# Kernel tuning notes

Hardware: AMD Instinct MI355X
Metric: run time of the kernel (lower is better)

The kernel has to match this reference:

```python
import jax, jax.numpy as jnp
import numpy as np

B, T, C, HD = 4, 2048, 1024, 64

def setup_inputs() -> dict:
    key = jax.random.key(0)
    kx, kq, kk, kv = jax.random.split(key, 4)
    # Weights stored as [n_embed, head_size]; equivalent to torch Linear weight transposed.
    scale = 1.0 / np.sqrt(C)
    return {
        "x": jax.random.normal(kx, (B, T, C), dtype=jnp.float32),
        "Wq": jax.random.normal(kq, (C, HD), dtype=jnp.float32) * scale,
        "Wk": jax.random.normal(kk, (C, HD), dtype=jnp.float32) * scale,
        "Wv": jax.random.normal(kv, (C, HD), dtype=jnp.float32) * scale,
    }

def reference(x, Wq, Wk, Wv):
    # Projections (no bias)
    q = x @ Wq  # [B,T,HD]
    k = x @ Wk
    v = x @ Wv
    hd = k.shape[-1]
    # NOTE: original multiplies by sqrt(head_size) (not the usual 1/sqrt) -- faithful.
    scores = jnp.einsum("btd,bsd->bts", q, k) * (hd ** 0.5)  # [B,T,T]
    # First softmax over full (unmasked) rows
    w = jax.nn.softmax(scores, axis=-1)
    # Causal mask applied AFTER the first softmax, then a second softmax
    causal = jnp.tril(jnp.ones((q.shape[1], q.shape[1]), dtype=bool))  # [T,T]
    w = jnp.where(causal[None, :, :], w, -jnp.inf)
    w = jax.nn.softmax(w, axis=-1)
    out = jnp.einsum("bts,bsd->btd", w, v)  # [B,T,HD]
    return out
```

## Files before the change

### kernel.cpp

```cpp
#include <hip/hip_runtime.h>
#include <math.h>

#define T_  2048
#define C_  1024
#define HD_ 64

typedef __attribute__((ext_vector_type(8))) short bf16x8;
typedef __attribute__((ext_vector_type(4))) float f32x4;

#define MFMA_BF16(A, B, C) __builtin_amdgcn_mfma_f32_16x16x32_bf16(A, B, C, 0, 0, 0)

__device__ __forceinline__ short f2bf(float f) {
    union { float f; unsigned u; } v; v.f = f;
    unsigned r = v.u + 0x7fffu + ((v.u >> 16) & 1u);
    return (short)(r >> 16);
}
__device__ __forceinline__ float bf2f(short s) {
    union { float f; unsigned u; } v;
    v.u = ((unsigned)(unsigned short)s) << 16;
    return v.f;
}

__global__ __launch_bounds__(256) void prep_w_kernel(
    const float* __restrict__ Wq, const float* __restrict__ Wk,
    const float* __restrict__ Wv, short* __restrict__ wt)
{
    const int m = blockIdx.y;
    const float* W = (m == 0) ? Wq : (m == 1) ? Wk : Wv;
    const int t = threadIdx.x;
    const int c = blockIdx.x * 64 + (t >> 2);
    const int hg = (t & 3) * 16;
    const float4* wp = (const float4*)(W + (size_t)c * HD_ + hg);
    short* hi = wt + (size_t)(m * 2 + 0) * 64 * 1024;
    short* lo = wt + (size_t)(m * 2 + 1) * 64 * 1024;
    #pragma unroll
    for (int u = 0; u < 4; ++u) {
        float4 f = wp[u];
        float vs[4] = {f.x, f.y, f.z, f.w};
        #pragma unroll
        for (int e = 0; e < 4; ++e) {
            int h = hg + u * 4 + e;
            short hh = f2bf(vs[e]);
            hi[(size_t)h * 1024 + c] = hh;
            lo[(size_t)h * 1024 + c] = f2bf(vs[e] - bf2f(hh));
        }
    }
}

__global__ __launch_bounds__(256) void qkv_proj_kernel(
    const float* __restrict__ x, const short* __restrict__ wt,
    short* __restrict__ qhp, short* __restrict__ qlp,
    short* __restrict__ khp, short* __restrict__ klp,
    short* __restrict__ vtp)
{
    __shared__ __align__(16) short xh[32 * 64], xl[32 * 64];
    __shared__ __align__(16) short wh[192 * 64], wl[192 * 64];

    const int t = threadIdx.x, L = t & 63, wv = t >> 6;
    const int R0 = blockIdx.x * 32;
    const int xrow = t >> 3, xch = t & 7;

    f32x4 acc[2][3];
    #pragma unroll
    for (int i = 0; i < 2; ++i)
        #pragma unroll
        for (int j = 0; j < 3; ++j) acc[i][j] = {0.f, 0.f, 0.f, 0.f};

    float4 xa0, xa1;
    bf16x8 wr[2][6];
    const float* xp = x + (size_t)(R0 + xrow) * C_ + xch * 8;

    auto loadX = [&](int c0) {
        xa0 = *(const float4*)(xp + c0);
        xa1 = *(const float4*)(xp + c0 + 4);
    };
    auto loadW = [&](int c0) {
        #pragma unroll
        for (int pl = 0; pl < 2; ++pl)
            #pragma unroll
            for (int u = 0; u < 6; ++u) {
                int cc = t + 256 * u;
                int row = cc >> 3, ch = cc & 7;
                int m = row >> 6, h = row & 63;
                wr[pl][u] = *(const bf16x8*)(wt + (size_t)(m * 2 + pl) * 65536
                                             + (size_t)h * 1024 + c0 + ch * 8);
            }
    };

    loadX(0); loadW(0);
    for (int c0 = 0; c0 < C_; c0 += 64) {
        __syncthreads();
        {
            float vs[8] = {xa0.x, xa0.y, xa0.z, xa0.w, xa1.x, xa1.y, xa1.z, xa1.w};
            bf16x8 vh, vl;
            #pragma unroll
            for (int e = 0; e < 8; ++e) {
                short hh = f2bf(vs[e]);
                vh[e] = hh;
                vl[e] = f2bf(vs[e] - bf2f(hh));
            }
            int slot = (xch ^ (xrow & 7)) * 8;
            *(bf16x8*)&xh[xrow * 64 + slot] = vh;
            *(bf16x8*)&xl[xrow * 64 + slot] = vl;
        }
        {
            #pragma unroll
            for (int pl = 0; pl < 2; ++pl)
                #pragma unroll
                for (int u = 0; u < 6; ++u) {
                    int cc = t + 256 * u;
                    int row = cc >> 3, ch = cc & 7;
                    short* dst = pl ? wl : wh;
                    *(bf16x8*)&dst[row * 64 + ((ch ^ (row & 7)) * 8)] = wr[pl][u];
                }
        }
        if (c0 + 64 < C_) { loadX(c0 + 64); loadW(c0 + 64); }
        __syncthreads();
        #pragma unroll
        for (int kc = 0; kc < 2; ++kc) {
            const int ch = kc * 4 + (L >> 4);
            bf16x8 axh[2], axl[2], bwh[3], bwl[3];
            #pragma unroll
            for (int rt = 0; rt < 2; ++rt) {
                int row = rt * 16 + (L & 15);
                int off = row * 64 + ((ch ^ (row & 7)) * 8);
                axh[rt] = *(const bf16x8*)&xh[off];
                axl[rt] = *(const bf16x8*)&xl[off];
            }
            #pragma unroll
            for (int cl = 0; cl < 3; ++cl) {
                int ct = wv + cl * 4;
                int wrow = ct * 16 + (L & 15);
                int off = wrow * 64 + ((ch ^ (wrow & 7)) * 8);
                bwh[cl] = *(const bf16x8*)&wh[off];
                bwl[cl] = *(const bf16x8*)&wl[off];
            }
            #pragma unroll
            for (int rt = 0; rt < 2; ++rt) {
                acc[rt][0] = MFMA_BF16(axl[rt], bwh[0], acc[rt][0]);
                acc[rt][0] = MFMA_BF16(axh[rt], bwl[0], acc[rt][0]);
                acc[rt][0] = MFMA_BF16(axh[rt], bwh[0], acc[rt][0]);
                acc[rt][1] = MFMA_BF16(axl[rt], bwh[1], acc[rt][1]);
                acc[rt][1] = MFMA_BF16(axh[rt], bwl[1], acc[rt][1]);
                acc[rt][1] = MFMA_BF16(axh[rt], bwh[1], acc[rt][1]);
                acc[rt][2] = MFMA_BF16(bwh[2], axh[rt], acc[rt][2]);
            }
        }
    }

    const int quad = L >> 4;
    #pragma unroll
    for (int rt = 0; rt < 2; ++rt) {
        #pragma unroll
        for (int r = 0; r < 4; ++r) {
            int row = R0 + rt * 16 + quad * 4 + r;
            int h = wv * 16 + (L & 15);
            float vq = acc[rt][0][r] * 8.f;
            short hq = f2bf(vq);
            qhp[(size_t)row * HD_ + h] = hq;
            qlp[(size_t)row * HD_ + h] = f2bf(vq - bf2f(hq));
            float vk = acc[rt][1][r];
            short hk = f2bf(vk);
            khp[(size_t)row * HD_ + h] = hk;
            klp[(size_t)row * HD_ + h] = f2bf(vk - bf2f(hk));
            int d = wv * 16 + quad * 4 + r;
            int tt = R0 + rt * 16 + (L & 15);
            int bb = tt >> 11, tl = tt & (T_ - 1);
            vtp[(size_t)(bb * 64 + d) * T_ + tl] = f2bf(acc[rt][2][r]);
        }
    }
}

__global__ __launch_bounds__(256) void stats_kernel(
    const short* __restrict__ qhp, const short* __restrict__ qlp,
    const short* __restrict__ khp, const short* __restrict__ klp,
    float* __restrict__ pm, float* __restrict__ sc)
{
    __shared__ __align__(16) short khs[64 * 64], kls[64 * 64];
    __shared__ float red[4 * 64 * 2];

    const int t = threadIdx.x, L = t & 63, wv = t >> 6;
    const int bt = blockIdx.x, seg = blockIdx.y, b = blockIdx.z;
    const int R0 = bt * 64, S0 = seg * 256;

    bf16x8 qfh[4][2], qfl[4][2];
    #pragma unroll
    for (int rt = 0; rt < 4; ++rt)
        #pragma unroll
        for (int dc = 0; dc < 2; ++dc) {
            int row = R0 + rt * 16 + (L & 15);
            size_t off = ((size_t)b * T_ + row) * HD_ + dc * 32 + (L >> 4) * 8;
            qfh[rt][dc] = *(const bf16x8*)(qhp + off);
            qfl[rt][dc] = *(const bf16x8*)(qlp + off);
        }

    float ml[4][4], ll[4][4];
    #pragma unroll
    for (int rt = 0; rt < 4; ++rt)
        #pragma unroll
        for (int r = 0; r < 4; ++r) { ml[rt][r] = -1e30f; ll[rt][r] = 0.f; }

    const int pl = t >> 7, id = t & 127;
    const short* ksrc = pl ? klp : khp;
    short* kdst = pl ? kls : khs;
    bf16x8 kr[4];
    auto loadK = [&](int jt) {
        #pragma unroll
        for (int u = 0; u < 4; ++u) {
            int cid = id * 4 + u;
            int col = cid >> 3, ch = cid & 7;
            kr[u] = *(const bf16x8*)(ksrc
                + ((size_t)b * T_ + S0 + jt * 64 + col) * HD_ + ch * 8);
        }
    };

    loadK(0);
    for (int jt = 0; jt < 4; ++jt) {
        __syncthreads();
        #pragma unroll
        for (int u = 0; u < 4; ++u) {
            int cid = id * 4 + u;
            int col = cid >> 3, ch = cid & 7;
            *(bf16x8*)&kdst[col * 64 + ((ch ^ (col & 7)) * 8)] = kr[u];
        }
        __syncthreads();
        if (jt < 3) loadK(jt + 1);
        const int colL = wv * 16 + (L & 15);
        bf16x8 kf[2], kfl[2];
        #pragma unroll
        for (int dc = 0; dc < 2; ++dc) {
            int ch = dc * 4 + (L >> 4);
            int off = colL * 64 + ((ch ^ (colL & 7)) * 8);
            kf[dc]  = *(const bf16x8*)&khs[off];
            kfl[dc] = *(const bf16x8*)&kls[off];
        }
        const bool doStore = (S0 + jt * 64) <= (R0 + 63);
        #pragma unroll
        for (int rt = 0; rt < 4; ++rt) {
            f32x4 s = {0.f, 0.f, 0.f, 0.f};
            #pragma unroll
            for (int dc = 0; dc < 2; ++dc) {
                s = MFMA_BF16(qfl[rt][dc], kf[dc], s);
                s = MFMA_BF16(qfh[rt][dc], kfl[dc], s);
                s = MFMA_BF16(qfh[rt][dc], kf[dc], s);
            }
            if (doStore) {
                #pragma unroll
                for (int r = 0; r < 4; ++r) {
                    int row = R0 + rt * 16 + (L >> 4) * 4 + r;
                    sc[((size_t)b * T_ + row) * T_ + S0 + jt * 64 + colL] = s[r];
                }
            }
            #pragma unroll
            for (int r = 0; r < 4; ++r) {
                float mn = fmaxf(ml[rt][r], s[r]);
                ll[rt][r] = ll[rt][r] * __expf(ml[rt][r] - mn) + __expf(s[r] - mn);
                ml[rt][r] = mn;
            }
        }
    }
    #pragma unroll
    for (int off = 1; off < 16; off <<= 1)
        #pragma unroll
        for (int rt = 0; rt < 4; ++rt)
            #pragma unroll
            for (int r = 0; r < 4; ++r) {
                float mo = __shfl_xor(ml[rt][r], off, 64);
                float lo = __shfl_xor(ll[rt][r], off, 64);
                float mn = fmaxf(ml[rt][r], mo);
                ll[rt][r] = ll[rt][r] * __expf(ml[rt][r] - mn) + lo * __expf(mo - mn);
                ml[rt][r] = mn;
            }
    if ((L & 15) == 0) {
        #pragma unroll
        for (int rt = 0; rt < 4; ++rt)
            #pragma unroll
            for (int r = 0; r < 4; ++r) {
                int row = rt * 16 + (L >> 4) * 4 + r;
                red[(wv * 64 + row) * 2 + 0] = ml[rt][r];
                red[(wv * 64 + row) * 2 + 1] = ll[rt][r];
            }
    }
    __syncthreads();
    if (t < 64) {
        float M = red[t * 2], S = red[t * 2 + 1];
        #pragma unroll
        for (int w = 1; w < 4; ++w) {
            float mo = red[(w * 64 + t) * 2], lo = red[(w * 64 + t) * 2 + 1];
            float mn = fmaxf(M, mo);
            S = S * __expf(M - mn) + lo * __expf(mo - mn);
            M = mn;
        }
        size_t o = ((size_t)((b * 32 + bt) * 8 + seg) * 64 + t) * 2;
        pm[o] = M;
        pm[o + 1] = S;
    }
}

__global__ __launch_bounds__(256) void stat_merge_kernel(
    const float* __restrict__ pm, float* __restrict__ msp, float* __restrict__ ilp)
{
    int gid = blockIdx.x * 256 + threadIdx.x;
    int b = gid >> 11, rl = gid & 2047, bt = rl >> 6, rr = rl & 63;
    float M = -1e30f, S = 0.f;
    #pragma unroll
    for (int seg = 0; seg < 8; ++seg) {
        size_t o = ((size_t)((b * 32 + bt) * 8 + seg) * 64 + rr) * 2;
        float mo = pm[o], lo = pm[o + 1];
        float mn = fmaxf(M, mo);
        S = S * __expf(M - mn) + lo * __expf(mo - mn);
        M = mn;
    }
    msp[gid] = M;
    ilp[gid] = 1.f / S;
}

__global__ __launch_bounds__(256) void pv_kernel(
    const float* __restrict__ sc, const short* __restrict__ vtp,
    const float* __restrict__ msp, const float* __restrict__ ilp,
    float* __restrict__ out)
{
    __shared__ float ored[4][16][64];
    __shared__ float dred[4][16];

    const int t = threadIdx.x, L = t & 63, wv = t >> 6;
    const int b = blockIdx.x & 3;
    const int p = 127 - (blockIdx.x >> 2);
    const int T0 = p * 16;
    const int row = T0 + (L & 15);

    const float ms = msp[b * T_ + row];
    const float is = ilp[b * T_ + row];
    const float* srow = sc + ((size_t)b * T_ + row) * T_;
    const short* vb = vtp + (size_t)b * 64 * T_;
    const int nJ = (T0 + 143) >> 7;
    const int cq = (L >> 4) * 8;

    f32x4 ov[4];
    #pragma unroll
    for (int dt = 0; dt < 4; ++dt) ov[dt] = {0.f, 0.f, 0.f, 0.f};
    float dn = 0.f;

    for (int jt = 0; jt < nJ; ++jt) {
        const int c0 = jt * 128 + wv * 32 + cq;
        float4 s0 = *(const float4*)(srow + c0);
        float4 s1 = *(const float4*)(srow + c0 + 4);
        float vs[8] = {s0.x, s0.y, s0.z, s0.w, s1.x, s1.y, s1.z, s1.w};
        bf16x8 ef;
        #pragma unroll
        for (int e = 0; e < 8; ++e) {
            float pvv = __expf(vs[e] - ms) * is;
            float evv = (c0 + e <= row) ? __expf(pvv) : 0.f;
            dn += evv;
            ef[e] = f2bf(evv);
        }
        #pragma unroll
        for (int dt = 0; dt < 4; ++dt) {
            bf16x8 vf = *(const bf16x8*)(vb + (size_t)(dt * 16 + (L & 15)) * T_ + c0);
            ov[dt] = MFMA_BF16(ef, vf, ov[dt]);
        }
    }

    dn += __shfl_xor(dn, 16, 64);
    dn += __shfl_xor(dn, 32, 64);
    if (L < 16) dred[wv][L] = dn;
    #pragma unroll
    for (int dt = 0; dt < 4; ++dt)
        #pragma unroll
        for (int r = 0; r < 4; ++r)
            ored[wv][(L >> 4) * 4 + r][dt * 16 + (L & 15)] = ov[dt][r];
    __syncthreads();

    const int orow = t >> 4, d0 = (t & 15) * 4;
    float D = dred[0][orow] + dred[1][orow] + dred[2][orow] + dred[3][orow];
    float di = 1.f / D;
    float4 o;
    o.x = (ored[0][orow][d0 + 0] + ored[1][orow][d0 + 0]
         + ored[2][orow][d0 + 0] + ored[3][orow][d0 + 0]) * di;
    o.y = (ored[0][orow][d0 + 1] + ored[1][orow][d0 + 1]
         + ored[2][orow][d0 + 1] + ored[3][orow][d0 + 1]) * di;
    o.z = (ored[0][orow][d0 + 2] + ored[1][orow][d0 + 2]
         + ored[2][orow][d0 + 2] + ored[3][orow][d0 + 2]) * di;
    o.w = (ored[0][orow][d0 + 3] + ored[1][orow][d0 + 3]
         + ored[2][orow][d0 + 3] + ored[3][orow][d0 + 3]) * di;
    *(float4*)(out + ((size_t)b * T_ + T0 + orow) * HD_ + d0) = o;
}

extern "C" void kernel_launch(void* const* d_in, const int* in_sizes, int n_in,
                              void* d_out, int out_size, void* d_ws, size_t ws_size,
                              hipStream_t stream) {
    (void)in_sizes; (void)n_in; (void)out_size; (void)ws_size;
    const float* x  = (const float*)d_in[0];
    const float* Wq = (const float*)d_in[1];
    const float* Wk = (const float*)d_in[2];
    const float* Wv = (const float*)d_in[3];
    float* outp = (float*)d_out;

    char* ws = (char*)d_ws;
    short* wt  = (short*)ws;
    float* pm  = (float*)ws;
    float* msp = (float*)(ws + 524288);
    float* ilp = (float*)(ws + 557056);
    short* qh = (short*)(ws + 786432);
    short* ql = (short*)(ws + 786432 + 1048576);
    short* kh = (short*)(ws + 786432 + 2 * 1048576);
    short* kl = (short*)(ws + 786432 + 3 * 1048576);
    short* vt = (short*)(ws + 786432 + 4 * 1048576);
    float* sc = (float*)(ws + 8388608);

    prep_w_kernel<<<dim3(16, 3), 256, 0, stream>>>(Wq, Wk, Wv, wt);
    qkv_proj_kernel<<<dim3(256), 256, 0, stream>>>(x, wt, qh, ql, kh, kl, vt);
    stats_kernel<<<dim3(32, 8, 4), 256, 0, stream>>>(qh, ql, kh, kl, pm, sc);
    stat_merge_kernel<<<dim3(32), 256, 0, stream>>>(pm, msp, ilp);
    pv_kernel<<<dim3(512), 256, 0, stream>>>(sc, vt, msp, ilp, outp);
}
```

Measured before the change: 148.9 us.

## Pre-swizzle weights into MFMA fragment layout, drop LDS staging, fuse stat merge

Weights are pre-laid out in prep_w into per-lane MFMA fragment order, so the projection kernel loads them straight into registers with 512 threads and no LDS weight tile. The stats kernel reads K fragments directly from global memory with double-buffered registers, which removes the LDS staging and its barriers. The separate stat-merge kernel is folded into pv_kernel, which saves one launch, and pv blocks are reordered to balance causal work. The cost is more global traffic from redundant fragment loads and higher register pressure.

```diff
diff --git a/kernel.cpp b/kernel.cpp
--- a/kernel.cpp
+++ b/kernel.cpp
@@ -23,151 +23,138 @@
 
 __global__ __launch_bounds__(256) void prep_w_kernel(
     const float* __restrict__ Wq, const float* __restrict__ Wk,
-    const float* __restrict__ Wv, short* __restrict__ wt)
+    const float* __restrict__ Wv, short* __restrict__ wtf)
 {
     const int m = blockIdx.y;
     const float* W = (m == 0) ? Wq : (m == 1) ? Wk : Wv;
     const int t = threadIdx.x;
     const int c = blockIdx.x * 64 + (t >> 2);
     const int hg = (t & 3) * 16;
+    const int ct = m * 4 + (t & 3);
+    const int c0i = c >> 6, kc = (c >> 5) & 1, lq = (c >> 3) & 3, e = c & 7;
     const float4* wp = (const float4*)(W + (size_t)c * HD_ + hg);
-    short* hi = wt + (size_t)(m * 2 + 0) * 64 * 1024;
-    short* lo = wt + (size_t)(m * 2 + 1) * 64 * 1024;
     #pragma unroll
     for (int u = 0; u < 4; ++u) {
         float4 f = wp[u];
         float vs[4] = {f.x, f.y, f.z, f.w};
         #pragma unroll
-        for (int e = 0; e < 4; ++e) {
-            int h = hg + u * 4 + e;
-            short hh = f2bf(vs[e]);
-            hi[(size_t)h * 1024 + c] = hh;
-            lo[(size_t)h * 1024 + c] = f2bf(vs[e] - bf2f(hh));
-        }
-    }
-}
-
-__global__ __launch_bounds__(256) void qkv_proj_kernel(
-    const float* __restrict__ x, const short* __restrict__ wt,
+        for (int ei = 0; ei < 4; ++ei) {
+            int h16 = u * 4 + ei;
+            int L = h16 + 16 * lq;
+            short hh = f2bf(vs[ei]);
+            short lo = f2bf(vs[ei] - bf2f(hh));
+            size_t oh = ((((size_t)(ct * 2 + 0) * 16 + c0i) * 2 + kc) * 64 + L) * 8 + e;
+            size_t ol = ((((size_t)(ct * 2 + 1) * 16 + c0i) * 2 + kc) * 64 + L) * 8 + e;
+            wtf[oh] = hh;
+            wtf[ol] = lo;
+        }
+    }
+}
+
+__global__ __launch_bounds__(512) void qkv_proj_kernel(
+    const float* __restrict__ x, const short* __restrict__ wtf,
     short* __restrict__ qhp, short* __restrict__ qlp,
     short* __restrict__ khp, short* __restrict__ klp,
     short* __restrict__ vtp)
 {
     __shared__ __align__(16) short xh[32 * 64], xl[32 * 64];
-    __shared__ __align__(16) short wh[192 * 64], wl[192 * 64];
 
     const int t = threadIdx.x, L = t & 63, wv = t >> 6;
     const int R0 = blockIdx.x * 32;
-    const int xrow = t >> 3, xch = t & 7;
-
-    f32x4 acc[2][3];
-    #pragma unroll
-    for (int i = 0; i < 2; ++i)
-        #pragma unroll
-        for (int j = 0; j < 3; ++j) acc[i][j] = {0.f, 0.f, 0.f, 0.f};
-
-    float4 xa0, xa1;
-    bf16x8 wr[2][6];
-    const float* xp = x + (size_t)(R0 + xrow) * C_ + xch * 8;
-
-    auto loadX = [&](int c0) {
-        xa0 = *(const float4*)(xp + c0);
-        xa1 = *(const float4*)(xp + c0 + 4);
+    const int rtb = (wv >> 2) * 16;
+    const int ctq = wv & 3;
+
+    f32x4 acc[3];
+    #pragma unroll
+    for (int j = 0; j < 3; ++j) acc[j] = {0.f, 0.f, 0.f, 0.f};
+
+    const int xrow = t >> 4, xc4 = t & 15;
+    const float* xp = x + (size_t)(R0 + xrow) * C_ + xc4 * 4;
+    float4 xa;
+    auto loadX = [&](int c0) { xa = *(const float4*)(xp + c0); };
+
+    const size_t lo8 = (size_t)L * 8;
+    auto loadWF = [&](int c0i, int kc, bf16x8* w) {
+        w[0] = *(const bf16x8*)(wtf + (size_t)((((ctq + 0) * 2 + 0) * 16 + c0i) * 2 + kc) * 512 + lo8);
+        w[1] = *(const bf16x8*)(wtf + (size_t)((((ctq + 0) * 2 + 1) * 16 + c0i) * 2 + kc) * 512 + lo8);
+        w[2] = *(const bf16x8*)(wtf + (size_t)((((ctq + 4) * 2 + 0) * 16 + c0i) * 2 + kc) * 512 + lo8);
+        w[3] = *(const bf16x8*)(wtf + (size_t)((((ctq + 4) * 2 + 1) * 16 + c0i) * 2 + kc) * 512 + lo8);
+        w[4] = *(const bf16x8*)(wtf + (size_t)((((ctq + 8) * 2 + 0) * 16 + c0i) * 2 + kc) * 512 + lo8);
     };
-    auto loadW = [&](int c0) {
-        #pragma unroll
-        for (int pl = 0; pl < 2; ++pl)
-            #pragma unroll
-            for (int u = 0; u < 6; ++u) {
-                int cc = t + 256 * u;
-                int row = cc >> 3, ch = cc & 7;
-                int m = row >> 6, h = row & 63;
-                wr[pl][u] = *(const bf16x8*)(wt + (size_t)(m * 2 + pl) * 65536
-                                             + (size_t)h * 1024 + c0 + ch * 8);
-            }
-    };
-
-    loadX(0); loadW(0);
-    for (int c0 = 0; c0 < C_; c0 += 64) {
+
+    bf16x8 wf0[5], wf1[5];
+    loadX(0);
+    loadWF(0, 0, wf0);
+
+    const int c8 = xc4 >> 1, xhalf = xc4 & 1;
+    const int arow = rtb + (L & 15);
+
+    for (int c0i = 0; c0i < 16; ++c0i) {
         __syncthreads();
         {
-            float vs[8] = {xa0.x, xa0.y, xa0.z, xa0.w, xa1.x, xa1.y, xa1.z, xa1.w};
-            bf16x8 vh, vl;
-            #pragma unroll
-            for (int e = 0; e < 8; ++e) {
+            float vs[4] = {xa.x, xa.y, xa.z, xa.w};
+            short4 vh, vl;
+            short* vhp = (short*)&vh; short* vlp = (short*)&vl;
+            #pragma unroll
+            for (int e = 0; e < 4; ++e) {
                 short hh = f2bf(vs[e]);
-                vh[e] = hh;
-                vl[e] = f2bf(vs[e] - bf2f(hh));
-            }
-            int slot = (xch ^ (xrow & 7)) * 8;
-            *(bf16x8*)&xh[xrow * 64 + slot] = vh;
-            *(bf16x8*)&xl[xrow * 64 + slot] = vl;
-        }
+                vhp[e] = hh;
+                vlp[e] = f2bf(vs[e] - bf2f(hh));
+            }
+            int slot = xrow * 64 + ((c8 ^ (xrow & 7)) * 8) + xhalf * 4;
+            *(short4*)&xh[slot] = vh;
+            *(short4*)&xl[slot] = vl;
+        }
+        if (c0i < 15) loadX((c0i + 1) * 64);
+        __syncthreads();
+
+        loadWF(c0i, 1, wf1);
         {
-            #pragma unroll
-            for (int pl = 0; pl < 2; ++pl)
-                #pragma unroll
-                for (int u = 0; u < 6; ++u) {
-                    int cc = t + 256 * u;
-                    int row = cc >> 3, ch = cc & 7;
-                    short* dst = pl ? wl : wh;
-                    *(bf16x8*)&dst[row * 64 + ((ch ^ (row & 7)) * 8)] = wr[pl][u];
-                }
-        }
-        if (c0 + 64 < C_) { loadX(c0 + 64); loadW(c0 + 64); }
-        __syncthreads();
-        #pragma unroll
-        for (int kc = 0; kc < 2; ++kc) {
-            const int ch = kc * 4 + (L >> 4);
-            bf16x8 axh[2], axl[2], bwh[3], bwl[3];
-            #pragma unroll
-            for (int rt = 0; rt < 2; ++rt) {
-                int row = rt * 16 + (L & 15);
-                int off = row * 64 + ((ch ^ (row & 7)) * 8);
-                axh[rt] = *(const bf16x8*)&xh[off];
-                axl[rt] = *(const bf16x8*)&xl[off];
-            }
-            #pragma unroll
-            for (int cl = 0; cl < 3; ++cl) {
-                int ct = wv + cl * 4;
-                int wrow = ct * 16 + (L & 15);
-                int off = wrow * 64 + ((ch ^ (wrow & 7)) * 8);
-                bwh[cl] = *(const bf16x8*)&wh[off];
-                bwl[cl] = *(const bf16x8*)&wl[off];
-            }
-            #pragma unroll
-            for (int rt = 0; rt < 2; ++rt) {
-                acc[rt][0] = MFMA_BF16(axl[rt], bwh[0], acc[rt][0]);
-                acc[rt][0] = MFMA_BF16(axh[rt], bwl[0], acc[rt][0]);
-                acc[rt][0] = MFMA_BF16(axh[rt], bwh[0], acc[rt][0]);
-                acc[rt][1] = MFMA_BF16(axl[rt], bwh[1], acc[rt][1]);
-                acc[rt][1] = MFMA_BF16(axh[rt], bwl[1], acc[rt][1]);
-                acc[rt][1] = MFMA_BF16(axh[rt], bwh[1], acc[rt][1]);
-                acc[rt][2] = MFMA_BF16(bwh[2], axh[rt], acc[rt][2]);
-            }
+            int ch = 0 * 4 + (L >> 4);
+            int off = arow * 64 + ((ch ^ (arow & 7)) * 8);
+            bf16x8 axh = *(const bf16x8*)&xh[off];
+            bf16x8 axl = *(const bf16x8*)&xl[off];
+            acc[0] = MFMA_BF16(axl, wf0[0], acc[0]);
+            acc[0] = MFMA_BF16(axh, wf0[1], acc[0]);
+            acc[0] = MFMA_BF16(axh, wf0[0], acc[0]);
+            acc[1] = MFMA_BF16(axl, wf0[2], acc[1]);
+            acc[1] = MFMA_BF16(axh, wf0[3], acc[1]);
+            acc[1] = MFMA_BF16(axh, wf0[2], acc[1]);
+            acc[2] = MFMA_BF16(wf0[4], axh, acc[2]);
+        }
+        if (c0i < 15) loadWF(c0i + 1, 0, wf0);
+        {
+            int ch = 1 * 4 + (L >> 4);
+            int off = arow * 64 + ((ch ^ (arow & 7)) * 8);
+            bf16x8 axh = *(const bf16x8*)&xh[off];
+            bf16x8 axl = *(const bf16x8*)&xl[off];
+            acc[0] = MFMA_BF16(axl, wf1[0], acc[0]);
+            acc[0] = MFMA_BF16(axh, wf1[1], acc[0]);
+            acc[0] = MFMA_BF16(axh, wf1[0], acc[0]);
+            acc[1] = MFMA_BF16(axl, wf1[2], acc[1]);
+            acc[1] = MFMA_BF16(axh, wf1[3], acc[1]);
+            acc[1] = MFMA_BF16(axh, wf1[2], acc[1]);
+            acc[2] = MFMA_BF16(wf1[4], axh, acc[2]);
         }
     }
 
     const int quad = L >> 4;
     #pragma unroll
-    for (int rt = 0; rt < 2; ++rt) {
-        #pragma unroll
-        for (int r = 0; r < 4; ++r) {
-            int row = R0 + rt * 16 + quad * 4 + r;
-            int h = wv * 16 + (L & 15);
-            float vq = acc[rt][0][r] * 8.f;
-            short hq = f2bf(vq);
-            qhp[(size_t)row * HD_ + h] = hq;
-            qlp[(size_t)row * HD_ + h] = f2bf(vq - bf2f(hq));
-            float vk = acc[rt][1][r];
-            short hk = f2bf(vk);
-            khp[(size_t)row * HD_ + h] = hk;
-            klp[(size_t)row * HD_ + h] = f2bf(vk - bf2f(hk));
-            int d = wv * 16 + quad * 4 + r;
-            int tt = R0 + rt * 16 + (L & 15);
-            int bb = tt >> 11, tl = tt & (T_ - 1);
-            vtp[(size_t)(bb * 64 + d) * T_ + tl] = f2bf(acc[rt][2][r]);
-        }
+    for (int r = 0; r < 4; ++r) {
+        int row = R0 + rtb + quad * 4 + r;
+        int h = ctq * 16 + (L & 15);
+        float vq = acc[0][r] * 8.f;
+        short hq = f2bf(vq);
+        qhp[(size_t)row * HD_ + h] = hq;
+        qlp[(size_t)row * HD_ + h] = f2bf(vq - bf2f(hq));
+        float vk = acc[1][r];
+        short hk = f2bf(vk);
+        khp[(size_t)row * HD_ + h] = hk;
+        klp[(size_t)row * HD_ + h] = f2bf(vk - bf2f(hk));
+        int d = ctq * 16 + quad * 4 + r;
+        int tt = R0 + rtb + (L & 15);
+        int bb = tt >> 11, tl = tt & (T_ - 1);
+        vtp[(size_t)(bb * 64 + d) * T_ + tl] = f2bf(acc[2][r]);
     }
 }
 
@@ -176,7 +163,6 @@
     const short* __restrict__ khp, const short* __restrict__ klp,
     float* __restrict__ pm, float* __restrict__ sc)
 {
-    __shared__ __align__(16) short khs[64 * 64], kls[64 * 64];
     __shared__ float red[4 * 64 * 2];
 
     const int t = threadIdx.x, L = t & 63, wv = t >> 6;
@@ -200,49 +186,34 @@
         #pragma unroll
         for (int r = 0; r < 4; ++r) { ml[rt][r] = -1e30f; ll[rt][r] = 0.f; }
 
-    const int pl = t >> 7, id = t & 127;
-    const short* ksrc = pl ? klp : khp;
-    short* kdst = pl ? kls : khs;
-    bf16x8 kr[4];
-    auto loadK = [&](int jt) {
-        #pragma unroll
-        for (int u = 0; u < 4; ++u) {
-            int cid = id * 4 + u;
-            int col = cid >> 3, ch = cid & 7;
-            kr[u] = *(const bf16x8*)(ksrc
-                + ((size_t)b * T_ + S0 + jt * 64 + col) * HD_ + ch * 8);
+    const int colL = wv * 16 + (L & 15);
+    const short* kbh = khp + ((size_t)b * T_ + S0 + colL) * HD_;
+    const short* kbl = klp + ((size_t)b * T_ + S0 + colL) * HD_;
+    const int cho = (L >> 4) * 8;
+
+    bf16x8 kfh[2][2], kfl[2][2];
+    auto loadK = [&](int jt, bf16x8 kh[2], bf16x8 kl[2]) {
+        #pragma unroll
+        for (int dc = 0; dc < 2; ++dc) {
+            kh[dc] = *(const bf16x8*)(kbh + (size_t)jt * 64 * HD_ + dc * 32 + cho);
+            kl[dc] = *(const bf16x8*)(kbl + (size_t)jt * 64 * HD_ + dc * 32 + cho);
         }
     };
-
-    loadK(0);
+    loadK(0, kfh[0], kfl[0]);
+
+    #pragma unroll
     for (int jt = 0; jt < 4; ++jt) {
-        __syncthreads();
-        #pragma unroll
-        for (int u = 0; u < 4; ++u) {
-            int cid = id * 4 + u;
-            int col = cid >> 3, ch = cid & 7;
-            *(bf16x8*)&kdst[col * 64 + ((ch ^ (col & 7)) * 8)] = kr[u];
-        }
-        __syncthreads();
-        if (jt < 3) loadK(jt + 1);
-        const int colL = wv * 16 + (L & 15);
-        bf16x8 kf[2], kfl[2];
-        #pragma unroll
-        for (int dc = 0; dc < 2; ++dc) {
-            int ch = dc * 4 + (L >> 4);
-            int off = colL * 64 + ((ch ^ (colL & 7)) * 8);
-            kf[dc]  = *(const bf16x8*)&khs[off];
-            kfl[dc] = *(const bf16x8*)&kls[off];
-        }
+        const int cb = jt & 1;
+        if (jt < 3) loadK(jt + 1, kfh[cb ^ 1], kfl[cb ^ 1]);
         const bool doStore = (S0 + jt * 64) <= (R0 + 63);
         #pragma unroll
         for (int rt = 0; rt < 4; ++rt) {
             f32x4 s = {0.f, 0.f, 0.f, 0.f};
             #pragma unroll
             for (int dc = 0; dc < 2; ++dc) {
-                s = MFMA_BF16(qfl[rt][dc], kf[dc], s);
-                s = MFMA_BF16(qfh[rt][dc], kfl[dc], s);
-                s = MFMA_BF16(qfh[rt][dc], kf[dc], s);
+                s = MFMA_BF16(qfl[rt][dc], kfh[cb][dc], s);
+                s = MFMA_BF16(qfh[rt][dc], kfl[cb][dc], s);
+                s = MFMA_BF16(qfh[rt][dc], kfh[cb][dc], s);
             }
             if (doStore) {
                 #pragma unroll
@@ -297,40 +268,40 @@
     }
 }
 
-__global__ __launch_bounds__(256) void stat_merge_kernel(
-    const float* __restrict__ pm, float* __restrict__ msp, float* __restrict__ ilp)
-{
-    int gid = blockIdx.x * 256 + threadIdx.x;
-    int b = gid >> 11, rl = gid & 2047, bt = rl >> 6, rr = rl & 63;
-    float M = -1e30f, S = 0.f;
-    #pragma unroll
-    for (int seg = 0; seg < 8; ++seg) {
-        size_t o = ((size_t)((b * 32 + bt) * 8 + seg) * 64 + rr) * 2;
-        float mo = pm[o], lo = pm[o + 1];
-        float mn = fmaxf(M, mo);
-        S = S * __expf(M - mn) + lo * __expf(mo - mn);
-        M = mn;
-    }
-    msp[gid] = M;
-    ilp[gid] = 1.f / S;
-}
-
 __global__ __launch_bounds__(256) void pv_kernel(
     const float* __restrict__ sc, const short* __restrict__ vtp,
-    const float* __restrict__ msp, const float* __restrict__ ilp,
-    float* __restrict__ out)
+    const float* __restrict__ pm, float* __restrict__ out)
 {
     __shared__ float ored[4][16][64];
     __shared__ float dred[4][16];
+    __shared__ float msl[16], isl[16];
 
     const int t = threadIdx.x, L = t & 63, wv = t >> 6;
     const int b = blockIdx.x & 3;
-    const int p = 127 - (blockIdx.x >> 2);
+    const int i = blockIdx.x >> 2;
+    const int p = (i < 64) ? (127 - i) : (i - 64);
     const int T0 = p * 16;
+
+    if (t < 16) {
+        int row = T0 + t;
+        int bt = row >> 6, rr = row & 63;
+        float M = -1e30f, S = 0.f;
+        #pragma unroll
+        for (int seg = 0; seg < 8; ++seg) {
+            size_t o = ((size_t)((b * 32 + bt) * 8 + seg) * 64 + rr) * 2;
+            float mo = pm[o], lo = pm[o + 1];
+            float mn = fmaxf(M, mo);
+            S = S * __expf(M - mn) + lo * __expf(mo - mn);
+            M = mn;
+        }
+        msl[t] = M;
+        isl[t] = 1.f / S;
+    }
+    __syncthreads();
+
     const int row = T0 + (L & 15);
-
-    const float ms = msp[b * T_ + row];
-    const float is = ilp[b * T_ + row];
+    const float ms = msl[L & 15];
+    const float is = isl[L & 15];
     const float* srow = sc + ((size_t)b * T_ + row) * T_;
     const short* vb = vtp + (size_t)b * 64 * T_;
     const int nJ = (T0 + 143) >> 7;
@@ -399,8 +370,6 @@
     char* ws = (char*)d_ws;
     short* wt  = (short*)ws;
     float* pm  = (float*)ws;
-    float* msp = (float*)(ws + 524288);
-    float* ilp = (float*)(ws + 557056);
     short* qh = (short*)(ws + 786432);
     short* ql = (short*)(ws + 786432 + 1048576);
     short* kh = (short*)(ws + 786432 + 2 * 1048576);
@@ -409,8 +378,7 @@
     float* sc = (float*)(ws + 8388608);
 
     prep_w_kernel<<<dim3(16, 3), 256, 0, stream>>>(Wq, Wk, Wv, wt);
-    qkv_proj_kernel<<<dim3(256), 256, 0, stream>>>(x, wt, qh, ql, kh, kl, vt);
+    qkv_proj_kernel<<<dim3(256), 512, 0, stream>>>(x, wt, qh, ql, kh, kl, vt);
     stats_kernel<<<dim3(32, 8, 4), 256, 0, stream>>>(qh, ql, kh, kl, pm, sc);
-    stat_merge_kernel<<<dim3(32), 256, 0, stream>>>(pm, msp, ilp);
-    pv_kernel<<<dim3(512), 256, 0, stream>>>(sc, vt, msp, ilp, outp);
-}
+    pv_kernel<<<dim3(512), 256, 0, stream>>>(sc, vt, pm, outp);
+}
```

Result: faster. 139.9 us (-6.0%).
